# Optimization experiments

Hardware: AMD Instinct MI355X
Metric: run time of the kernel (lower is better)

The kernel has to match this reference:

```python
import jax, jax.numpy as jnp
import numpy as np

NUM_HEADS = 16

def setup_inputs() -> dict:
    key = jax.random.key(0)
    x = jax.random.normal(key, (4, 2048, 1024), dtype=jnp.float32)
    return {"x": x}

def reference(x) -> jnp.ndarray:
    B, T, D = x.shape
    H = NUM_HEADS
    hd = D // H
    xh = x.reshape(B, T, H, hd)                      # [B,T,H,hd]
    x_centered = xh - jnp.mean(xh, axis=1, keepdims=True)
    # mean-centered QK^T: [B,H,T,T]
    corr = jnp.einsum('bthd,bThd->bhtT', x_centered, x_centered)
    corr = jax.nn.softmax(corr, axis=-1)
    # weighted sum with UNcentered values
    out = jnp.einsum('bhtT,bThd->bthd', corr, xh)    # [B,T,H,hd]
    return out.reshape(B, T, D)
```

## Files before the change

kernel.cpp:

```cpp
#include <hip/hip_runtime.h>
#include <stdint.h>

#define B_   4
#define T_   2048
#define H_   16
#define HD_  64
#define D_   1024
#define QB   128
#define KB   64
#define NSTEP (T_ / KB)
#define L2E   1.44269504088896f
#define SQL2E 1.20112240878645f
#define THR2  15.5f
#define M2INIT 28.8539f
#define SKIPTHR (-24.5f)

typedef __attribute__((ext_vector_type(4)))  float    f32x4;
typedef __attribute__((ext_vector_type(16))) float    f32x16;
typedef __attribute__((ext_vector_type(8)))  _Float16 f16x8;
typedef __attribute__((ext_vector_type(2)))  __fp16   h16x2;

__device__ __forceinline__ f32x4 mfma16(f16x8 a, f16x8 b, f32x4 c) {
  return __builtin_amdgcn_mfma_f32_16x16x32_f16(a, b, c, 0, 0, 0);
}
__device__ __forceinline__ f32x16 mfma32(f16x8 a, f16x8 b, f32x16 c) {
  return __builtin_amdgcn_mfma_f32_32x32x16_f16(a, b, c, 0, 0, 0);
}
__device__ __forceinline__ f32x16 zero16() {
  f32x16 z;
  #pragma unroll
  for (int i = 0; i < 16; ++i) z[i] = 0.f;
  return z;
}
__device__ __forceinline__ float fexp2(float x) {
#if __has_builtin(__builtin_amdgcn_exp2f)
  return __builtin_amdgcn_exp2f(x);
#else
  return exp2f(x);
#endif
}
__device__ __forceinline__ uint32_t pkrtz_u(float a, float b) {
  h16x2 r = __builtin_amdgcn_cvt_pkrtz(a, b);
  return __builtin_bit_cast(uint32_t, r);
}
__device__ __forceinline__ float fdot2_u(uint32_t a, h16x2 ones, float c) {
  return __builtin_amdgcn_fdot2(__builtin_bit_cast(h16x2, a), ones, c, false);
}
__device__ __forceinline__ void pl32swap(uint32_t& a, uint32_t& b) {
  asm volatile("v_permlane32_swap_b32 %0, %1" : "+v"(a), "+v"(b));
}
__device__ __forceinline__ f16x8 mk_frag(uint32_t u0, uint32_t u1,
                                         uint32_t u2, uint32_t u3) {
  union { uint32_t u[4]; f16x8 v; } x;
  x.u[0] = u0; x.u[1] = u1; x.u[2] = u2; x.u[3] = u3;
  return x.v;
}
__device__ __forceinline__ void gld16(const void* g, void* l) {
  __builtin_amdgcn_global_load_lds(
      (const __attribute__((address_space(1))) uint32_t*)g,
      (__attribute__((address_space(3))) uint32_t*)l, 16, 0, 0);
}

__global__ __launch_bounds__(256)
void colmean_kernel(const float* __restrict__ x, float* __restrict__ mu) {
  const int b   = blockIdx.x >> 6;
  const int c0  = (blockIdx.x & 63) << 4;
  const int col = threadIdx.x & 15;
  const int rg  = threadIdx.x >> 4;
  const float* p = x + ((size_t)(b * T_ + rg * 128)) * D_ + c0 + col;
  float s = 0.f;
  #pragma unroll 8
  for (int r = 0; r < 128; ++r) s += p[(size_t)r * D_];
  __shared__ float red[16][17];
  red[rg][col] = s;
  __syncthreads();
  if (rg == 0) {
    float t = 0.f;
    #pragma unroll
    for (int i = 0; i < 16; ++i) t += red[i][col];
    mu[b * D_ + c0 + col] = t * (1.f / (float)T_);
  }
}

__global__ __launch_bounds__(256)
void cvt2_kernel(const float* __restrict__ x, const float* __restrict__ mu,
                 _Float16* __restrict__ KT, _Float16* __restrict__ VT) {
  const int unit = blockIdx.x * 4 + (threadIdx.x >> 6);
  const int bh   = unit >> 5;
  const int tile = unit & 31;
  const int b    = bh >> 4;
  const int h    = bh & 15;
  const int lane = threadIdx.x & 63;
  const int t    = tile * 64 + lane;

  const float* xr  = x  + ((size_t)(b * T_ + t)) * D_ + h * HD_;
  const float* mur = mu + b * D_ + h * HD_;

  _Float16 cfV[64];
  _Float16 cfK[64];
  #pragma unroll
  for (int u = 0; u < 16; ++u) {
    float4 f = *(const float4*)(xr + u * 4);
    float4 m = *(const float4*)(mur + u * 4);
    float c0 = f.x - m.x, c1 = f.y - m.y, c2 = f.z - m.z, c3 = f.w - m.w;
    cfV[u*4+0] = (_Float16)c0; cfK[u*4+0] = (_Float16)(c0 * SQL2E);
    cfV[u*4+1] = (_Float16)c1; cfK[u*4+1] = (_Float16)(c1 * SQL2E);
    cfV[u*4+2] = (_Float16)c2; cfK[u*4+2] = (_Float16)(c2 * SQL2E);
    cfV[u*4+3] = (_Float16)c3; cfK[u*4+3] = (_Float16)(c3 * SQL2E);
  }
  _Float16* kt = KT + ((size_t)(bh * 32 + tile)) * 4096;
  #pragma unroll
  for (int g = 0; g < 8; ++g)
    *(f16x8*)&kt[g * 512 + lane * 8] = *(const f16x8*)&cfK[g * 8];
  _Float16* vt = VT + ((size_t)(bh * 32 + tile)) * 4096 + (lane >> 3) * 512 + (lane & 7);
  #pragma unroll
  for (int d = 0; d < 64; ++d) vt[d * 8] = cfV[d];
}

__global__ __launch_bounds__(256, 4)
void attn13_kernel(const _Float16* __restrict__ KT,
                   const _Float16* __restrict__ VT,
                   const float* __restrict__ mu,
                   float* __restrict__ out) {
  __shared__ __align__(16) _Float16 Kb[4][4096];

  const int tid  = threadIdx.x;
  const int lane = tid & 63;
  const int wv   = tid >> 6;
  const int c    = lane & 31;
  const int hp   = lane >> 5;

  const int bid = blockIdx.x;
  const int wid = (bid & 7) * 128 + (bid >> 3);
  const int qb  = wid & 15;
  const int bh  = wid >> 4;
  const int b   = bh >> 4;
  const int h   = bh & 15;

  const int q0w = qb * QB + wv * 32;
  const int start = 2 * qb;

  f16x8 qf[4];
  {
    const _Float16* qt = KT + ((size_t)(bh * 32 + (q0w >> 6))) * 4096;
    const int qrow = ((wv & 1) * 32) + c;
    #pragma unroll
    for (int s = 0; s < 4; ++s)
      qf[s] = *(const f16x8*)&qt[(2 * s + hp) * 512 + qrow * 8];
  }

  const char* kbase = (const char*)KT + ((size_t)(bh * 32)) * 8192 + wv * 2048 + lane * 16;
  const int fb = hp * 512 + c * 8;

  const _Float16* vfrag = VT + ((size_t)(bh * 32)) * 4096 + fb;

  f32x16 acc0 = zero16(), acc1 = zero16();
  f32x16 C1 = zero16();
  #pragma unroll
  for (int i = 0; i < 16; ++i) C1[i] = -M2INIT;
  float lrun = 0.f;
  h16x2 one2; one2[0] = (__fp16)1.0f; one2[1] = (__fp16)1.0f;

  #pragma unroll
  for (int t = 0; t < 3; ++t) {
    const char* sp = kbase + (size_t)((start + t) & 31) * 8192;
    gld16(sp,        &Kb[t][wv * 1024]);
    gld16(sp + 1024, &Kb[t][wv * 1024 + 512]);
  }
  __builtin_amdgcn_sched_barrier(0);
  asm volatile("s_waitcnt vmcnt(4)" ::: "memory");
  __builtin_amdgcn_s_barrier();
  __builtin_amdgcn_sched_barrier(0);

  for (int i = 0; i < NSTEP; ++i) {
    if (i + 3 < NSTEP) {
      const char* sp = kbase + (size_t)((start + i + 3) & 31) * 8192;
      gld16(sp,        &Kb[(i + 3) & 3][wv * 1024]);
      gld16(sp + 1024, &Kb[(i + 3) & 3][wv * 1024 + 512]);
    }
    const _Float16* Kp = &Kb[i & 3][fb];
    const _Float16* Vp = vfrag + (size_t)((start + i) & 31) * 4096;

    #pragma unroll
    for (int kt = 0; kt < 2; ++kt) {
      f32x16 st;
      __builtin_amdgcn_s_setprio(1);
      st = mfma32(*(const f16x8*)&Kp[0 * 1024 + kt * 256], qf[0], C1);
      st = mfma32(*(const f16x8*)&Kp[1 * 1024 + kt * 256], qf[1], st);
      st = mfma32(*(const f16x8*)&Kp[2 * 1024 + kt * 256], qf[2], st);
      st = mfma32(*(const f16x8*)&Kp[3 * 1024 + kt * 256], qf[3], st);
      __builtin_amdgcn_s_setprio(0);

      float n0 = fmaxf(fmaxf(st[0],  st[1]),  st[2]);
      float n1 = fmaxf(fmaxf(st[3],  st[4]),  st[5]);
      float n2 = fmaxf(fmaxf(st[6],  st[7]),  st[8]);
      float n3 = fmaxf(fmaxf(st[9],  st[10]), st[11]);
      float n4 = fmaxf(fmaxf(st[12], st[13]), st[14]);
      float pm = fmaxf(fmaxf(fmaxf(n0, n1), fmaxf(n2, n3)), fmaxf(n4, st[15]));

      if (__all(pm <= SKIPTHR)) continue;

      const float pmw = fmaxf(pm, __shfl_xor(pm, 32));
      if (!__all(pm <= THR2)) {
        const float dm  = fmaxf(pmw, 0.f);
        const float al  = fexp2(-dm);
        lrun *= al;
        #pragma unroll
        for (int ii = 0; ii < 16; ++ii) { C1[ii] -= dm; st[ii] -= dm; }
        #pragma unroll
        for (int rr = 0; rr < 16; ++rr) {
          const int row = (rr & 3) + 8 * (rr >> 2) + 4 * hp;
          const float a = __shfl(al, row);
          acc0[rr] *= a; acc1[rr] *= a;
        }
      }

      f16x8 v0a = *(const f16x8*)&Vp[(2*kt    ) * 1024      ];
      f16x8 v1a = *(const f16x8*)&Vp[(2*kt + 1) * 1024      ];
      f16x8 v0b = *(const f16x8*)&Vp[(2*kt    ) * 1024 + 256];
      f16x8 v1b = *(const f16x8*)&Vp[(2*kt + 1) * 1024 + 256];

      f16x8 paL, paH;
      float rsA = 0.f, rsB = 0.f;
      #pragma unroll
      for (int v = 0; v < 2; ++v) {
        uint32_t A0 = pkrtz_u(fexp2(st[8*v+0]), fexp2(st[8*v+1]));
        uint32_t A1 = pkrtz_u(fexp2(st[8*v+2]), fexp2(st[8*v+3]));
        uint32_t B0 = pkrtz_u(fexp2(st[8*v+4]), fexp2(st[8*v+5]));
        uint32_t B1 = pkrtz_u(fexp2(st[8*v+6]), fexp2(st[8*v+7]));
        rsA = fdot2_u(A0, one2, rsA); rsA = fdot2_u(A1, one2, rsA);
        rsB = fdot2_u(B0, one2, rsB); rsB = fdot2_u(B1, one2, rsB);
        pl32swap(A0, B0);
        pl32swap(A1, B1);
        if (v == 0) paL = mk_frag(A0, A1, B0, B1);
        else        paH = mk_frag(A0, A1, B0, B1);
      }
      lrun += rsA + rsB;

      __builtin_amdgcn_s_setprio(1);
      acc0 = mfma32(paL, v0a, acc0);
      acc0 = mfma32(paH, v1a, acc0);
      acc1 = mfma32(paL, v0b, acc1);
      acc1 = mfma32(paH, v1b, acc1);
      __builtin_amdgcn_s_setprio(0);
    }

    if (i + 1 < NSTEP) {
      __builtin_amdgcn_sched_barrier(0);
      if      (i + 3 < NSTEP) asm volatile("s_waitcnt vmcnt(4)" ::: "memory");
      else if (i + 2 < NSTEP) asm volatile("s_waitcnt vmcnt(2)" ::: "memory");
      else                    asm volatile("s_waitcnt vmcnt(0)" ::: "memory");
      __builtin_amdgcn_s_barrier();
      __builtin_amdgcn_sched_barrier(0);
    }
  }

  const float ltot = lrun + __shfl_xor(lrun, 32);
  const float linv = 1.0f / ltot;
  const float mv0 = mu[b * D_ + h * HD_ + c];
  const float mv1 = mu[b * D_ + h * HD_ + 32 + c];
  #pragma unroll
  for (int r = 0; r < 16; ++r) {
    const int row = (r & 3) + 8 * (r >> 2) + 4 * hp;
    const float lr = __shfl(linv, row);
    const int q = q0w + row;
    float* orow = out + (size_t)(b * T_ + q) * D_ + h * HD_;
    orow[c]      = acc0[r] * lr + mv0;
    orow[32 + c] = acc1[r] * lr + mv1;
  }
}

__global__ __launch_bounds__(256)
void attn_fb_kernel(const float* __restrict__ x, const float* __restrict__ mu,
                    float* __restrict__ out) {
  __shared__ __align__(16) _Float16 Kt[64 * 64];
  __shared__ __align__(16) _Float16 Vt[64 * 64];
  __shared__ __align__(16) _Float16 Pl[4][2][16 * 64];

  const int tid  = threadIdx.x;
  const int lane = tid & 63;
  const int wv   = tid >> 6;
  const int j    = lane & 15;
  const int g    = lane >> 4;

  const int qb = blockIdx.x & 15;
  const int bh = blockIdx.x >> 4;
  const int b  = bh >> 4;
  const int h  = bh & 15;

  const float* xb  = x  + (size_t)b * T_ * D_;
  const float* muh = mu + b * D_ + h * HD_;

  f16x8 qf[2][2];
  const int q0 = qb * 128 + wv * 32;
  #pragma unroll
  for (int qt = 0; qt < 2; ++qt) {
    const float* qrow = xb + (size_t)(q0 + qt * 16 + j) * D_ + h * HD_;
    #pragma unroll
    for (int ks = 0; ks < 2; ++ks) {
      const int d0 = ks * 32 + g * 8;
      float4 a  = *(const float4*)(qrow + d0);
      float4 cc = *(const float4*)(qrow + d0 + 4);
      float4 m0 = *(const float4*)(muh + d0);
      float4 m1 = *(const float4*)(muh + d0 + 4);
      f16x8 f;
      f[0] = (_Float16)(a.x - m0.x); f[1] = (_Float16)(a.y - m0.y);
      f[2] = (_Float16)(a.z - m0.z); f[3] = (_Float16)(a.w - m0.w);
      f[4] = (_Float16)(cc.x - m1.x); f[5] = (_Float16)(cc.y - m1.y);
      f[6] = (_Float16)(cc.z - m1.z); f[7] = (_Float16)(cc.w - m1.w);
      qf[qt][ks] = f;
    }
  }

  const int kd0 = (tid & 7) * 8;
  const float4 kmu0 = *(const float4*)(muh + kd0);
  const float4 kmu1 = *(const float4*)(muh + kd0 + 4);
  const int vd2 = (tid & 31) * 2;
  const int vkc = tid >> 5;

  f32x4 acc[2][4];
  float mrun[2][4], lrun[2][4];
  #pragma unroll
  for (int qt = 0; qt < 2; ++qt) {
    #pragma unroll
    for (int n = 0; n < 4; ++n) acc[qt][n] = f32x4{0.f, 0.f, 0.f, 0.f};
    #pragma unroll
    for (int r = 0; r < 4; ++r) { mrun[qt][r] = -1e30f; lrun[qt][r] = 0.f; }
  }

  const int swj = (j & 7) << 3;

  for (int step = 0; step < NSTEP; ++step) {
    const size_t krow0 = (size_t)(step * KB) * D_ + h * HD_;
    __syncthreads();

    #pragma unroll
    for (int cc2 = 0; cc2 < 2; ++cc2) {
      const int kk = (tid >> 3) + cc2 * 32;
      const float* src = xb + krow0 + (size_t)kk * D_ + kd0;
      float4 a = *(const float4*)src;
      float4 cc = *(const float4*)(src + 4);
      f16x8 f;
      f[0] = (_Float16)(a.x - kmu0.x); f[1] = (_Float16)(a.y - kmu0.y);
      f[2] = (_Float16)(a.z - kmu0.z); f[3] = (_Float16)(a.w - kmu0.w);
      f[4] = (_Float16)(cc.x - kmu1.x); f[5] = (_Float16)(cc.y - kmu1.y);
      f[6] = (_Float16)(cc.z - kmu1.z); f[7] = (_Float16)(cc.w - kmu1.w);
      *(f16x8*)&Kt[kk * 64 + (kd0 ^ ((kk & 7) << 3))] = f;
    }
    {
      float2 t[8];
      #pragma unroll
      for (int e = 0; e < 8; ++e)
        t[e] = *(const float2*)(xb + krow0 + (size_t)(vkc * 8 + e) * D_ + vd2);
      f16x8 f0, f1;
      #pragma unroll
      for (int e = 0; e < 8; ++e) { f0[e] = (_Float16)t[e].x; f1[e] = (_Float16)t[e].y; }
      *(f16x8*)&Vt[(vd2    ) * 64 + ((vkc * 8) ^ (((vd2    ) & 7) << 3))] = f0;
      *(f16x8*)&Vt[(vd2 + 1) * 64 + ((vkc * 8) ^ (((vd2 + 1) & 7) << 3))] = f1;
    }
    __syncthreads();

    f32x4 s[2][4];
    #pragma unroll
    for (int n = 0; n < 4; ++n) {
      const int rb = (n * 16 + j) * 64;
      f16x8 kb0 = *(const f16x8*)&Kt[rb + (((     g * 8)) ^ swj)];
      f16x8 kb1 = *(const f16x8*)&Kt[rb + (((32 + g * 8)) ^ swj)];
      #pragma unroll
      for (int qt = 0; qt < 2; ++qt) {
        f32x4 z = f32x4{0.f, 0.f, 0.f, 0.f};
        z = mfma16(qf[qt][0], kb0, z);
        s[qt][n] = mfma16(qf[qt][1], kb1, z);
      }
    }

    #pragma unroll
    for (int qt = 0; qt < 2; ++qt) {
      float al[4];
      #pragma unroll
      for (int r = 0; r < 4; ++r) {
        float v = fmaxf(fmaxf(s[qt][0][r], s[qt][1][r]),
                        fmaxf(s[qt][2][r], s[qt][3][r]));
        v = fmaxf(v, __shfl_xor(v, 1, 16));
        v = fmaxf(v, __shfl_xor(v, 2, 16));
        v = fmaxf(v, __shfl_xor(v, 4, 16));
        v = fmaxf(v, __shfl_xor(v, 8, 16));
        const float mn = fmaxf(mrun[qt][r], v);
        al[r] = exp2f((mrun[qt][r] - mn) * L2E);
        mrun[qt][r] = mn;
        float p0 = exp2f((s[qt][0][r] - mn) * L2E);
        float p1 = exp2f((s[qt][1][r] - mn) * L2E);
        float p2 = exp2f((s[qt][2][r] - mn) * L2E);
        float p3 = exp2f((s[qt][3][r] - mn) * L2E);
        float rs = (p0 + p1) + (p2 + p3);
        rs += __shfl_xor(rs, 1, 16);
        rs += __shfl_xor(rs, 2, 16);
        rs += __shfl_xor(rs, 4, 16);
        rs += __shfl_xor(rs, 8, 16);
        lrun[qt][r] = lrun[qt][r] * al[r] + rs;
        const int q   = g * 4 + r;
        const int qsw = (q & 7) << 3;
        _Float16* prow = &Pl[wv][qt][q * 64];
        prow[(     j) ^ qsw] = (_Float16)p0;
        prow[(16 + j) ^ qsw] = (_Float16)p1;
        prow[(32 + j) ^ qsw] = (_Float16)p2;
        prow[(48 + j) ^ qsw] = (_Float16)p3;
      }
      #pragma unroll
      for (int n = 0; n < 4; ++n) {
        acc[qt][n][0] *= al[0]; acc[qt][n][1] *= al[1];
        acc[qt][n][2] *= al[2]; acc[qt][n][3] *= al[3];
      }
    }

    asm volatile("s_waitcnt lgkmcnt(0)" ::: "memory");

    f16x8 pa[2][2];
    #pragma unroll
    for (int qt = 0; qt < 2; ++qt) {
      const _Float16* Pw = &Pl[wv][qt][0];
      pa[qt][0] = *(const f16x8*)&Pw[j * 64 + (((     g * 8)) ^ swj)];
      pa[qt][1] = *(const f16x8*)&Pw[j * 64 + (((32 + g * 8)) ^ swj)];
    }
    #pragma unroll
    for (int n = 0; n < 4; ++n) {
      const int rb = (n * 16 + j) * 64;
      f16x8 v0 = *(const f16x8*)&Vt[rb + (((     g * 8)) ^ swj)];
      f16x8 v1 = *(const f16x8*)&Vt[rb + (((32 + g * 8)) ^ swj)];
      #pragma unroll
      for (int qt = 0; qt < 2; ++qt) {
        acc[qt][n] = mfma16(pa[qt][0], v0, acc[qt][n]);
        acc[qt][n] = mfma16(pa[qt][1], v1, acc[qt][n]);
      }
    }
  }

  #pragma unroll
  for (int qt = 0; qt < 2; ++qt) {
    float inv[4];
    #pragma unroll
    for (int r = 0; r < 4; ++r) inv[r] = 1.0f / lrun[qt][r];
    #pragma unroll
    for (int n = 0; n < 4; ++n) {
      #pragma unroll
      for (int r = 0; r < 4; ++r) {
        const int q = q0 + qt * 16 + g * 4 + r;
        out[(size_t)(b * T_ + q) * D_ + h * HD_ + n * 16 + j] =
            acc[qt][n][r] * inv[r];
      }
    }
  }
}

extern "C" void kernel_launch(void* const* d_in, const int* in_sizes, int n_in,
                              void* d_out, int out_size, void* d_ws, size_t ws_size,
                              hipStream_t stream) {
  (void)in_sizes; (void)n_in; (void)out_size;
  const float* x  = (const float*)d_in[0];
  float* outp     = (float*)d_out;

  const size_t MU_BYTES  = (size_t)B_ * D_ * sizeof(float);
  const size_t C16_BYTES = (size_t)B_ * T_ * D_ * 2;

  float* mu = (float*)d_ws;
  hipLaunchKernelGGL(colmean_kernel, dim3(B_ * 64), dim3(256), 0, stream, x, mu);

  if (ws_size >= MU_BYTES + 2 * C16_BYTES) {
    _Float16* KT = (_Float16*)((char*)d_ws + MU_BYTES);
    _Float16* VT = (_Float16*)((char*)d_ws + MU_BYTES + C16_BYTES);
    hipLaunchKernelGGL(cvt2_kernel, dim3(512), dim3(256), 0, stream, x, mu, KT, VT);
    hipLaunchKernelGGL(attn13_kernel, dim3((T_ / QB) * B_ * H_), dim3(256), 0, stream,
                       KT, VT, mu, outp);
  } else {
    hipLaunchKernelGGL(attn_fb_kernel, dim3((T_ / 128) * B_ * H_), dim3(256), 0, stream,
                       x, mu, outp);
  }
}
```

Baseline: 83.65 us.

## Load K fragments directly from global memory instead of LDS ring buffer

Removes the 4-stage shared-memory ring buffer for K tiles, along with its async global-to-LDS loads, waitcnt and block barriers. Each wave now reads its own K fragments straight from global memory into registers at the start of each step, the way V was already read. This drops per-step block-wide synchronization and LDS traffic. In exchange, K loads are no longer prefetched ahead, so global or L2 latency may be exposed, and all four waves fetch the same K data separately.

```diff
diff --git a/kernel.cpp b/kernel.cpp
--- a/kernel.cpp
+++ b/kernel.cpp
@@ -118,12 +118,10 @@
 }
 
 __global__ __launch_bounds__(256, 4)
-void attn13_kernel(const _Float16* __restrict__ KT,
+void attn14_kernel(const _Float16* __restrict__ KT,
                    const _Float16* __restrict__ VT,
                    const float* __restrict__ mu,
                    float* __restrict__ out) {
-  __shared__ __align__(16) _Float16 Kb[4][4096];
-
   const int tid  = threadIdx.x;
   const int lane = tid & 63;
   const int wv   = tid >> 6;
@@ -149,9 +147,8 @@
       qf[s] = *(const f16x8*)&qt[(2 * s + hp) * 512 + qrow * 8];
   }
 
-  const char* kbase = (const char*)KT + ((size_t)(bh * 32)) * 8192 + wv * 2048 + lane * 16;
   const int fb = hp * 512 + c * 8;
-
+  const _Float16* kfrag = KT + ((size_t)(bh * 32)) * 4096 + fb;
   const _Float16* vfrag = VT + ((size_t)(bh * 32)) * 4096 + fb;
 
   f32x16 acc0 = zero16(), acc1 = zero16();
@@ -161,34 +158,28 @@
   float lrun = 0.f;
   h16x2 one2; one2[0] = (__fp16)1.0f; one2[1] = (__fp16)1.0f;
 
-  #pragma unroll
-  for (int t = 0; t < 3; ++t) {
-    const char* sp = kbase + (size_t)((start + t) & 31) * 8192;
-    gld16(sp,        &Kb[t][wv * 1024]);
-    gld16(sp + 1024, &Kb[t][wv * 1024 + 512]);
-  }
-  __builtin_amdgcn_sched_barrier(0);
-  asm volatile("s_waitcnt vmcnt(4)" ::: "memory");
-  __builtin_amdgcn_s_barrier();
-  __builtin_amdgcn_sched_barrier(0);
-
   for (int i = 0; i < NSTEP; ++i) {
-    if (i + 3 < NSTEP) {
-      const char* sp = kbase + (size_t)((start + i + 3) & 31) * 8192;
-      gld16(sp,        &Kb[(i + 3) & 3][wv * 1024]);
-      gld16(sp + 1024, &Kb[(i + 3) & 3][wv * 1024 + 512]);
-    }
-    const _Float16* Kp = &Kb[i & 3][fb];
-    const _Float16* Vp = vfrag + (size_t)((start + i) & 31) * 4096;
+    const size_t sidx = (size_t)((start + i) & 31);
+    const _Float16* Kp = kfrag + sidx * 4096;
+    const _Float16* Vp = vfrag + sidx * 4096;
+
+    f16x8 k00 = *(const f16x8*)&Kp[0 * 1024      ];
+    f16x8 k01 = *(const f16x8*)&Kp[1 * 1024      ];
+    f16x8 k02 = *(const f16x8*)&Kp[2 * 1024      ];
+    f16x8 k03 = *(const f16x8*)&Kp[3 * 1024      ];
+    f16x8 k10 = *(const f16x8*)&Kp[0 * 1024 + 256];
+    f16x8 k11 = *(const f16x8*)&Kp[1 * 1024 + 256];
+    f16x8 k12 = *(const f16x8*)&Kp[2 * 1024 + 256];
+    f16x8 k13 = *(const f16x8*)&Kp[3 * 1024 + 256];
 
     #pragma unroll
     for (int kt = 0; kt < 2; ++kt) {
       f32x16 st;
       __builtin_amdgcn_s_setprio(1);
-      st = mfma32(*(const f16x8*)&Kp[0 * 1024 + kt * 256], qf[0], C1);
-      st = mfma32(*(const f16x8*)&Kp[1 * 1024 + kt * 256], qf[1], st);
-      st = mfma32(*(const f16x8*)&Kp[2 * 1024 + kt * 256], qf[2], st);
-      st = mfma32(*(const f16x8*)&Kp[3 * 1024 + kt * 256], qf[3], st);
+      st = mfma32(kt ? k10 : k00, qf[0], C1);
+      st = mfma32(kt ? k11 : k01, qf[1], st);
+      st = mfma32(kt ? k12 : k02, qf[2], st);
+      st = mfma32(kt ? k13 : k03, qf[3], st);
       __builtin_amdgcn_s_setprio(0);
 
       float n0 = fmaxf(fmaxf(st[0],  st[1]),  st[2]);
@@ -243,15 +234,6 @@
       acc1 = mfma32(paL, v0b, acc1);
       acc1 = mfma32(paH, v1b, acc1);
       __builtin_amdgcn_s_setprio(0);
-    }
-
-    if (i + 1 < NSTEP) {
-      __builtin_amdgcn_sched_barrier(0);
-      if      (i + 3 < NSTEP) asm volatile("s_waitcnt vmcnt(4)" ::: "memory");
-      else if (i + 2 < NSTEP) asm volatile("s_waitcnt vmcnt(2)" ::: "memory");
-      else                    asm volatile("s_waitcnt vmcnt(0)" ::: "memory");
-      __builtin_amdgcn_s_barrier();
-      __builtin_amdgcn_sched_barrier(0);
     }
   }
 
@@ -469,7 +451,7 @@
     _Float16* KT = (_Float16*)((char*)d_ws + MU_BYTES);
     _Float16* VT = (_Float16*)((char*)d_ws + MU_BYTES + C16_BYTES);
     hipLaunchKernelGGL(cvt2_kernel, dim3(512), dim3(256), 0, stream, x, mu, KT, VT);
-    hipLaunchKernelGGL(attn13_kernel, dim3((T_ / QB) * B_ * H_), dim3(256), 0, stream,
+    hipLaunchKernelGGL(attn14_kernel, dim3((T_ / QB) * B_ * H_), dim3(256), 0, stream,
                        KT, VT, mu, outp);
   } else {
     hipLaunchKernelGGL(attn_fb_kernel, dim3((T_ / 128) * B_ * H_), dim3(256), 0, stream,
```

Result: slower. 90.28 us (+7.9%).
